# Optimization experiments

Hardware: AMD Instinct MI355X
Metric: run time of the kernel (lower is better)

## Reference

```python
import jax, jax.numpy as jnp
import numpy as np

B, T, V, ION, N = 16, 32, 26, 8, 500
U, E, H = 64, 512, 512
CIN = V * ION + 1  # 209


def setup_inputs() -> dict:
    key = jax.random.key(0)
    ks = jax.random.split(key, 40)
    s = 0.05
    inp = {
        "location_index": jax.random.uniform(ks[0], (B, T, V, ION), jnp.float32),
        "peaks_location": jax.random.uniform(ks[1], (B, N), jnp.float32),
        "peaks_intensity": jax.random.uniform(ks[2], (B, N), jnp.float32),
        "aa_input": jax.random.randint(ks[3], (B, T), 0, V),
        "h0": jax.random.normal(ks[4], (1, B, H), jnp.float32) * 0.1,
        "c0": jax.random.normal(ks[5], (1, B, H), jnp.float32) * 0.1,
        "dsf": jnp.zeros((), jnp.float32),
        "conv1_w": jax.random.normal(ks[6], (U, CIN), jnp.float32) * s,
        "conv1_b": jnp.zeros((U,), jnp.float32),
        "conv2_w": jax.random.normal(ks[7], (2 * U, U), jnp.float32) * s,
        "conv2_b": jnp.zeros((2 * U,), jnp.float32),
        "conv3_w": jax.random.normal(ks[8], (4 * U, 2 * U), jnp.float32) * s,
        "conv3_b": jnp.zeros((4 * U,), jnp.float32),
        "fc1_w": jax.random.normal(ks[9], (2 * U, 4 * U), jnp.float32) * s,
        "fc1_b": jnp.zeros((2 * U,), jnp.float32),
        "fc2_w": jax.random.normal(ks[10], (U, 2 * U), jnp.float32) * s,
        "fc2_b": jnp.zeros((U,), jnp.float32),
        "bn0_g": jnp.ones((CIN,), jnp.float32), "bn0_b": jnp.zeros((CIN,), jnp.float32),
        "bn1_g": jnp.ones((U,), jnp.float32), "bn1_b": jnp.zeros((U,), jnp.float32),
        "bn2_g": jnp.ones((2 * U,), jnp.float32), "bn2_b": jnp.zeros((2 * U,), jnp.float32),
        "bn3_g": jnp.ones((4 * U,), jnp.float32), "bn3_b": jnp.zeros((4 * U,), jnp.float32),
        "bn4_g": jnp.ones((2 * U,), jnp.float32), "bn4_b": jnp.zeros((2 * U,), jnp.float32),
        "bn5_g": jnp.ones((U,), jnp.float32), "bn5_b": jnp.zeros((U,), jnp.float32),
        "emb": jax.random.normal(ks[11], (V, E), jnp.float32) * s,
        "w_ih": jax.random.normal(ks[12], (4 * H, E), jnp.float32) * s,
        "w_hh": jax.random.normal(ks[13], (4 * H, H), jnp.float32) * s,
        "b_ih": jnp.zeros((4 * H,), jnp.float32),
        "b_hh": jnp.zeros((4 * H,), jnp.float32),
        "out_w": jax.random.normal(ks[14], (V, U + H), jnp.float32) * s,
        "out_b": jnp.zeros((V,), jnp.float32),
    }
    return inp


def _bn(x, g, b):
    # training-mode batch norm (biased variance), matches default torch module mode
    axes = (0, 2) if x.ndim == 3 else (0,)
    shp = (1, -1, 1) if x.ndim == 3 else (1, -1)
    m = jnp.mean(x, axes, keepdims=True)
    v = jnp.var(x, axes, keepdims=True)
    return (x - m) / jnp.sqrt(v + 1e-5) * g.reshape(shp) + b.reshape(shp)


def _forward(location_index, peaks_location, peaks_intensity, aa_input, h0, c0, dsf,
             conv1_w, conv1_b, conv2_w, conv2_b, conv3_w, conv3_b,
             fc1_w, fc1_b, fc2_w, fc2_b,
             bn0_g, bn0_b, bn1_g, bn1_b, bn2_g, bn2_b, bn3_g, bn3_b, bn4_g, bn4_b, bn5_g, bn5_b,
             emb, w_ih, w_hh, b_ih, b_hh, out_w, out_b):
    relu = jax.nn.relu
    pl = peaks_location[:, None, :, None]            # [B,1,N,1]
    pi = peaks_intensity[:, None, :, None]           # [B,1,N,1]
    li = location_index.reshape(B, T, 1, V * ION)    # [B,T,1,208]
    mp = (pl > 1e-5).astype(jnp.float32)
    ml = (li > 1e-5).astype(jnp.float32)
    ppm = (pl - li) / (li + 1e-6) * 1e6              # [B,T,N,208]
    feat = jnp.exp(-jnp.abs(ppm / 5.0 * jax.nn.sigmoid(dsf))) * mp * ml
    pi_b = jnp.broadcast_to(pi, (B, T, N, 1))
    x = jnp.concatenate([feat, pi_b], axis=3)        # [B,T,N,209]
    x = x.reshape(B * T, N, CIN).transpose(0, 2, 1)  # [BT,209,N]
    # TNet (1x1 convs are channel matmuls)
    x = _bn(x, bn0_g, bn0_b)
    x = relu(_bn(jnp.einsum('mcn,oc->mon', x, conv1_w) + conv1_b[:, None], bn1_g, bn1_b))
    x = relu(_bn(jnp.einsum('mcn,oc->mon', x, conv2_w) + conv2_b[:, None], bn2_g, bn2_b))
    x = relu(_bn(jnp.einsum('mcn,oc->mon', x, conv3_w) + conv3_b[:, None], bn3_g, bn3_b))
    x = jnp.max(x, axis=2)                            # [BT,4U]
    x = relu(_bn(x @ fc1_w.T + fc1_b, bn4_g, bn4_b))
    x = relu(_bn(x @ fc2_w.T + fc2_b, bn5_g, bn5_b))
    ion = x.reshape(B, T, U)
    # LSTM over aa embeddings (torch gate order i,f,g,o)
    xemb = emb[aa_input]                              # [B,T,E]
    def step(carry, xt):
        h, c = carry
        g = xt @ w_ih.T + b_ih + h @ w_hh.T + b_hh
        i, f, gg, o = jnp.split(g, 4, axis=1)
        c = jax.nn.sigmoid(f) * c + jax.nn.sigmoid(i) * jnp.tanh(gg)
        h = jax.nn.sigmoid(o) * jnp.tanh(c)
        return (h, c), h
    (hT, cT), hs = jax.lax.scan(step, (h0[0], c0[0]), xemb.transpose(1, 0, 2))
    lstm_out = hs.transpose(1, 0, 2)                  # [B,T,H]
    of = jnp.concatenate([ion, relu(lstm_out)], axis=2)  # dropout = identity (eval)
    logit = of @ out_w.T + out_b                      # [B,T,26]
    return logit, hT[None], cT[None]


def reference(location_index, peaks_location, peaks_intensity, aa_input, h0, c0, dsf,
              conv1_w, conv1_b, conv2_w, conv2_b, conv3_w, conv3_b,
              fc1_w, fc1_b, fc2_w, fc2_b,
              bn0_g, bn0_b, bn1_g, bn1_b, bn2_g, bn2_b, bn3_g, bn3_b, bn4_g, bn4_b, bn5_g, bn5_b,
              emb, w_ih, w_hh, b_ih, b_hh, out_w, out_b):
    return _forward(location_index, peaks_location, peaks_intensity, aa_input, h0, c0, dsf,
                    conv1_w, conv1_b, conv2_w, conv2_b, conv3_w, conv3_b,
                    fc1_w, fc1_b, fc2_w, fc2_b,
                    bn0_g, bn0_b, bn1_g, bn1_b, bn2_g, bn2_b, bn3_g, bn3_b, bn4_g, bn4_b, bn5_g, bn5_b,
                    emb, w_ih, w_hh, b_ih, b_hh, out_w, out_b)
```

## Files before the change

### kernel.cpp

```cpp
#include <hip/hip_runtime.h>
#include <hip/hip_bf16.h>
#include <math.h>

#define Bb 16
#define Tt 32
#define Vv 26
#define Nn 500
#define Uu 64
#define Hh 512
#define CIN 209
#define K1P 256
#define Mm 512
#define Rr 256000
#define NB1 4000
#define NB23 2000

typedef short short8 __attribute__((ext_vector_type(8)));
typedef float f32x4 __attribute__((ext_vector_type(4)));

__device__ __forceinline__ float sigf(float x){ return 1.0f/(1.0f+expf(-x)); }
__device__ __forceinline__ float frcp(float x){ return __builtin_amdgcn_rcpf(x); }
__device__ __forceinline__ unsigned short f2bf(float f){
  __hip_bfloat16 h = __float2bfloat16(f);
  return *reinterpret_cast<unsigned short*>(&h);
}
__device__ __forceinline__ float bf2f(unsigned short h){
  return __uint_as_float(((unsigned)h)<<16);
}

__global__ void k_front(const float* __restrict__ W2, const float* __restrict__ W3,
                        const float* __restrict__ EMB, const float* __restrict__ WIH,
                        const float* __restrict__ BIH, const float* __restrict__ BHH,
                        const float* __restrict__ L, const float* __restrict__ PL,
                        const float* __restrict__ PI, const float* __restrict__ DSF,
                        unsigned short* __restrict__ W2B, unsigned short* __restrict__ W3B,
                        unsigned short* __restrict__ W1B,
                        float* __restrict__ embw, float* __restrict__ ps0){
  int bid = blockIdx.x;
  int tid = threadIdx.x;
  if (bid < 172){
    int idx = bid*256 + tid;
    if (idx < 8192){ W2B[idx] = f2bf(W2[idx]); return; }
    idx -= 8192;
    if (idx < 32768){ W3B[idx] = f2bf(W3[idx]); return; }
    idx -= 32768;
    if (idx < 3008){ int oo = idx/47, kk = 209 + idx - (idx/47)*47; W1B[oo*K1P + kk] = 0; }
    return;
  }
  if (bid < 13484){
    int gw = (bid-172)*4 + (tid>>6);
    int lane = tid & 63;
    int v = gw >> 11;
    int j = gw & 2047;
    const float4* ea = (const float4*)&EMB[(size_t)v*512];
    const float4* wa = (const float4*)&WIH[(size_t)j*512];
    float4 e0 = ea[lane*2], e1 = ea[lane*2+1];
    float4 w0 = wa[lane*2], w1 = wa[lane*2+1];
    float s = e0.x*w0.x + e0.y*w0.y + e0.z*w0.z + e0.w*w0.w
            + e1.x*w1.x + e1.y*w1.y + e1.z*w1.z + e1.w*w1.w;
    #pragma unroll
    for (int off=1; off<64; off<<=1) s += __shfl_xor(s,off);
    if (lane==0) embw[(size_t)v*2048 + j] = s + BIH[j] + BHH[j];
    return;
  }
  int fid = bid - 13484;
  int m = fid>>3, q = fid&7;
  int b = m >> 5;
  int n0 = q*62 + ((q<4)?q:4);
  int cnt = 62 + (q<4 ? 1 : 0);
  __shared__ float pl_sh[63], pi_sh[63];
  for (int n=tid; n<cnt; n+=256){ pl_sh[n]=PL[b*Nn+n0+n]; pi_sh[n]=PI[b*Nn+n0+n]; }
  __syncthreads();
  if (tid >= CIN) return;
  float sum=0.f, sq=0.f;
  if (tid < CIN-1){
    float li = L[m*208 + tid];
    if (li > 1e-5f){
      float cfac = sigf(DSF[0])*200000.0f;
      float si = frcp(li + 1e-6f)*cfac;
      for (int n=0;n<cnt;n++){
        float pl = pl_sh[n];
        float f = (pl > 1e-5f) ? __expf(-fabsf((pl-li)*si)) : 0.f;
        sum += f; sq += f*f;
      }
    }
  } else {
    for (int n=0;n<cnt;n++){ float v=pi_sh[n]; sum+=v; sq+=v*v; }
  }
  int pb = m*8+q;
  ps0[(size_t)pb*CIN + tid] = sum;
  ps0[(size_t)(4096+pb)*CIN + tid] = sq;
}

__global__ void k_reduce0(const float* __restrict__ ps, const float* __restrict__ g,
                          const float* __restrict__ w1, unsigned short* __restrict__ w1b){
  int c = blockIdx.x;
  int tid = threadIdx.x;
  float s=0.f, q=0.f;
  for (int nb=tid; nb<4096; nb+=256){
    s += ps[(size_t)nb*CIN + c];
    q += ps[(size_t)(4096+nb)*CIN + c];
  }
  #pragma unroll
  for (int off=1; off<64; off<<=1){ s += __shfl_xor(s,off); q += __shfl_xor(q,off); }
  __shared__ float rs[4], rq[4];
  __shared__ float a_sh;
  if ((tid&63)==0){ rs[tid>>6]=s; rq[tid>>6]=q; }
  __syncthreads();
  if (tid==0){
    s = rs[0]+rs[1]+rs[2]+rs[3]; q = rq[0]+rq[1]+rq[2]+rq[3];
    float mean = s/(float)Rr;
    float var  = q/(float)Rr - mean*mean;
    a_sh = g[c]*rsqrtf(var + 1e-5f);
  }
  __syncthreads();
  if (tid < 64) w1b[tid*K1P + c] = f2bf(w1[tid*CIN + c] * a_sh);
}

__global__ void k_reduce_ps(const float* __restrict__ ps, int NB, int C, float invCount,
                            const float* __restrict__ g, const float* __restrict__ bt,
                            float* __restrict__ abb){
  int c = blockIdx.x;
  int tid = threadIdx.x;
  float s=0.f, q=0.f;
  for (int nb=tid; nb<NB; nb+=256){
    s += ps[(size_t)nb*C + c];
    q += ps[(size_t)(NB+nb)*C + c];
  }
  #pragma unroll
  for (int off=1; off<64; off<<=1){ s += __shfl_xor(s,off); q += __shfl_xor(q,off); }
  __shared__ float rs[4], rq[4];
  if ((tid&63)==0){ rs[tid>>6]=s; rq[tid>>6]=q; }
  __syncthreads();
  if (tid==0){
    s = rs[0]+rs[1]+rs[2]+rs[3]; q = rq[0]+rq[1]+rq[2]+rq[3];
    float mean = s*invCount;
    float var  = q*invCount - mean*mean;
    float istd = rsqrtf(var + 1e-5f);
    float a = g[c]*istd;
    abb[c] = a;
    abb[C+c] = bt[c] - mean*a;
  }
}

__global__ void k_colstats_par(const float* __restrict__ Z, int Mrows, int C,
                               const float* __restrict__ g, const float* __restrict__ bt,
                               float* __restrict__ abb){
  int c = blockIdx.x;
  int tid = threadIdx.x;
  float s=0.f,q=0.f;
  for (int r=tid; r<Mrows; r+=256){ float v=Z[(size_t)r*C+c]; s+=v; q+=v*v; }
  #pragma unroll
  for (int off=1; off<64; off<<=1){ s += __shfl_xor(s,off); q += __shfl_xor(q,off); }
  __shared__ float rs[4], rq[4];
  if ((tid&63)==0){ rs[tid>>6]=s; rq[tid>>6]=q; }
  __syncthreads();
  if (tid==0){
    s = rs[0]+rs[1]+rs[2]+rs[3]; q = rq[0]+rq[1]+rq[2]+rq[3];
    float mean = s/(float)Mrows;
    float var  = q/(float)Mrows - mean*mean;
    float istd = rsqrtf(var + 1e-5f);
    float a = g[c]*istd;
    abb[c]=a; abb[C+c]=bt[c]-mean*a;
  }
}

__launch_bounds__(256)
__global__ void k_conv1mf(const float* __restrict__ L, const float* __restrict__ PL,
                          const float* __restrict__ PI, const float* __restrict__ DSF,
                          const unsigned short* __restrict__ W1B,
                          unsigned short* __restrict__ Z1B, float* __restrict__ ps){
  __shared__ __align__(16) unsigned short Abuf[64*128];
  __shared__ __align__(16) unsigned short Bbuf[64*128];
  __shared__ __align__(16) float si_s[2][208];
  __shared__ float pl_s[64], pi_s[64];
  __shared__ int mi_i[64];
  __shared__ float red[4][2][64];
  int tid = threadIdx.x;
  int r0 = blockIdx.x*64;
  int m0 = r0/500, m1 = (r0+63)/500;
  float cfac = sigf(DSF[0])*200000.0f;
  if (tid < 64){
    int r = r0+tid; int m = r/500; int n = r - m*500; int b = m >> 5;
    pl_s[tid] = PL[b*Nn+n]; pi_s[tid] = PI[b*Nn+n]; mi_i[tid] = (m == m0) ? 0 : 1;
  }
  for (int j=tid; j<416; j+=256){
    int gg = (j>=208) ? 1 : 0; int jj = j - gg*208;
    float li = L[(size_t)(gg?m1:m0)*208 + jj];
    si_s[gg][jj] = (li > 1e-5f) ? frcp(li+1e-6f)*cfac : -1.0f;
  }
  int lane = tid&63, wid = tid>>6;
  int l15 = lane&15, lhi = lane>>4;
  int ar = wid*16 + l15;
  unsigned aswz = ((unsigned)(ar&7))<<4;
  f32x4 acc[4] = {};
  __syncthreads();
  for (int kc=0; kc<2; kc++){
    if (kc) __syncthreads();
    for (int e=tid; e<1024; e+=256){
      int row = e>>4; int k4 = (e&15)*8;
      short8 w = *(const short8*)&W1B[row*K1P + kc*128 + k4];
      unsigned byte = ((unsigned)(row*128 + k4))*2u ^ (((unsigned)(row&7))<<4);
      *(short8*)((char*)Bbuf + byte) = w;
    }
    for (int e=tid; e<1024; e+=256){
      int row = e>>4; int j0l = (e&15)*8;
      int jg = kc*128 + j0l;
      float pl = pl_s[row];
      bool plok = pl > 1e-5f;
      short8 st;
      if (jg < 208){
        int mi = mi_i[row];
        const float* lp = &L[(size_t)(mi?m1:m0)*208 + jg];
        float4 la = *(const float4*)lp;
        float4 lb = *(const float4*)(lp+4);
        float4 sa = *(const float4*)&si_s[mi][jg];
        float4 sb = *(const float4*)&si_s[mi][jg+4];
        float li[8] = {la.x,la.y,la.z,la.w,lb.x,lb.y,lb.z,lb.w};
        float si[8] = {sa.x,sa.y,sa.z,sa.w,sb.x,sb.y,sb.z,sb.w};
        #pragma unroll
        for (int j=0;j<8;j++){
          float v = (plok && si[j] >= 0.f) ? __expf(-fabsf((pl-li[j])*si[j])) : 0.f;
          st[j] = (short)f2bf(v);
        }
      } else {
        #pragma unroll
        for (int j=0;j<8;j++) st[j] = 0;
        if (jg == 208) st[0] = (short)f2bf(pi_s[row]);
      }
      unsigned byte = ((unsigned)(row*128 + j0l))*2u ^ (((unsigned)(row&7))<<4);
      *(short8*)((char*)Abuf + byte) = st;
    }
    __syncthreads();
    #pragma unroll
    for (int ks=0; ks<4; ks++){
      int kb = ks*32 + lhi*8;
      short8 af = *(const short8*)((const char*)Abuf + ((((unsigned)(ar*128 + kb))*2u) ^ aswz));
      #pragma unroll
      for (int fj=0; fj<4; fj++){
        int bc = fj*16 + l15;
        short8 bfv = *(const short8*)((const char*)Bbuf + ((((unsigned)(bc*128 + kb))*2u) ^ (((unsigned)(bc&7))<<4)));
        acc[fj] = __builtin_amdgcn_mfma_f32_16x16x32_bf16(af, bfv, acc[fj], 0, 0, 0);
      }
    }
  }
  #pragma unroll
  for (int fj=0; fj<4; fj++){
    int ch = fj*16 + l15;
    float s=0.f, q=0.f;
    #pragma unroll
    for (int qi=0; qi<4; qi++){
      float zv = acc[fj][qi];
      int rg = r0 + wid*16 + lhi*4 + qi;
      Z1B[(size_t)rg*Uu + ch] = f2bf(zv);
      s += zv; q = fmaf(zv,zv,q);
    }
    s += __shfl_xor(s,16); s += __shfl_xor(s,32);
    q += __shfl_xor(q,16); q += __shfl_xor(q,32);
    if (lhi == 0){ red[wid][0][ch]=s; red[wid][1][ch]=q; }
  }
  __syncthreads();
  if (tid < 64){
    float s = red[0][0][tid]+red[1][0][tid]+red[2][0][tid]+red[3][0][tid];
    float q = red[0][1][tid]+red[1][1][tid]+red[2][1][tid]+red[3][1][tid];
    ps[(size_t)blockIdx.x*Uu + tid] = s;
    ps[(size_t)(NB1 + blockIdx.x)*Uu + tid] = q;
  }
}

__launch_bounds__(256,4)
__global__ void k_convmf(const unsigned short* __restrict__ Xin, const float* __restrict__ abbIn,
                         const unsigned short* __restrict__ Wb,
                         unsigned short* __restrict__ Zout,
                         float* __restrict__ ps, int NB){
  constexpr int K = 64, Ctot = 128;
  __shared__ __align__(16) unsigned short Abuf[128*K];
  __shared__ float abbs[2*K];
  __shared__ float redS[2][128], redQ[2][128];
  int tid = threadIdx.x;
  int r0 = blockIdx.x*128;
  for (int e=tid; e<2*K; e+=256) abbs[e] = abbIn[e];
  __syncthreads();
  constexpr int CPR = K/8;
  for (int e=tid; e<128*CPR; e+=256){
    int row = e/CPR; int kc = (e - row*CPR)*8;
    short8 rawv = *(const short8*)(Xin + (size_t)(r0+row)*K + kc);
    short8 st;
    #pragma unroll
    for (int j=0;j<8;j++){
      float t = fmaxf(abbs[kc+j]*bf2f((unsigned short)rawv[j]) + abbs[K+kc+j], 0.f);
      st[j] = (short)f2bf(t);
    }
    unsigned byte = ((unsigned)(row*K + kc))*2u; byte ^= ((unsigned)(row&7))<<4;
    *(short8*)((char*)Abuf + byte) = st;
  }
  __syncthreads();

  int lane = tid&63, wid = tid>>6;
  int wr = wid>>1, wc = wid&1;
  int l15 = lane&15, lhi = lane>>4;
  f32x4 acc[4][4] = {};
  #pragma unroll
  for (int ks=0; ks<K/32; ks++){
    short8 af[4], bfr[4];
    int kb = ks*32 + lhi*8;
    #pragma unroll
    for (int f=0; f<4; f++){
      int arr = wr*64 + f*16 + l15;
      unsigned ab = ((unsigned)(arr*K + kb))*2u ^ (((unsigned)(arr&7))<<4);
      af[f] = *(const short8*)((const char*)Abuf + ab);
      int bc = wc*64 + f*16 + l15;
      bfr[f] = *(const short8*)&Wb[(size_t)bc*K + kb];
    }
    #pragma unroll
    for (int fi=0; fi<4; fi++)
      #pragma unroll
      for (int fj=0; fj<4; fj++)
        acc[fi][fj] = __builtin_amdgcn_mfma_f32_16x16x32_bf16(af[fi], bfr[fj], acc[fi][fj], 0, 0, 0);
  }

  #pragma unroll
  for (int fj=0; fj<4; fj++){
    int cg = wc*64 + fj*16 + l15;
    float s=0.f, q=0.f;
    #pragma unroll
    for (int fi=0; fi<4; fi++){
      #pragma unroll
      for (int qi=0; qi<4; qi++){
        float zv = acc[fi][fj][qi];
        int rg = r0 + wr*64 + fi*16 + lhi*4 + qi;
        Zout[(size_t)rg*Ctot + cg] = f2bf(zv);
        s += zv; q = fmaf(zv,zv,q);
      }
    }
    s += __shfl_xor(s,16); s += __shfl_xor(s,32);
    q += __shfl_xor(q,16); q += __shfl_xor(q,32);
    if (lhi == 0){ redS[wr][cg]=s; redQ[wr][cg]=q; }
  }
  __syncthreads();
  if (tid < 128){
    float s = redS[0][tid]+redS[1][tid];
    float q = redQ[0][tid]+redQ[1][tid];
    size_t ci = (size_t)blockIdx.x*Ctot + tid;
    ps[ci] = s;
    ps[(size_t)NB*Ctot + ci] = q;
  }
}

__launch_bounds__(256,3)
__global__ void k_conv3mf(const unsigned short* __restrict__ Xin, const float* __restrict__ abbIn,
                          const unsigned short* __restrict__ Wb,
                          float* __restrict__ ps, int NB,
                          float* __restrict__ pm, float* __restrict__ pn){
  constexpr int K = 128, Ctot = 256;
  __shared__ __align__(16) unsigned short Abuf[128*K];
  __shared__ float abbs[2*K];
  __shared__ float redS[2][128], redQ[2][128];
  __shared__ float mxS[2][2][128], mnS[2][2][128];
  int tid = threadIdx.x;
  int r0 = blockIdx.x*128;
  for (int e=tid; e<2*K; e+=256) abbs[e] = abbIn[e];
  __syncthreads();
  constexpr int CPR = K/8;
  for (int e=tid; e<128*CPR; e+=256){
    int row = e/CPR; int kc = (e - row*CPR)*8;
    short8 rawv = *(const short8*)(Xin + (size_t)(r0+row)*K + kc);
    short8 st;
    #pragma unroll
    for (int j=0;j<8;j++){
      float t = fmaxf(abbs[kc+j]*bf2f((unsigned short)rawv[j]) + abbs[K+kc+j], 0.f);
      st[j] = (short)f2bf(t);
    }
    unsigned byte = ((unsigned)(row*K + kc))*2u; byte ^= ((unsigned)(row&7))<<4;
    *(short8*)((char*)Abuf + byte) = st;
  }
  __syncthreads();

  int lane = tid&63, wid = tid>>6;
  int wr = wid>>1, wc = wid&1;
  int l15 = lane&15, lhi = lane>>4;
  int m0 = r0/500;
  int mhi = (m0+1)*500;
  bool onem = (r0+127) < mhi;

  for (int half=0; half<2; half++){
    int c0 = half*128;
    if (half) __syncthreads();

    f32x4 acc[4][4] = {};
    #pragma unroll
    for (int ks=0; ks<K/32; ks++){
      short8 af[4], bfr[4];
      int kb = ks*32 + lhi*8;
      #pragma unroll
      for (int f=0; f<4; f++){
        int arr = wr*64 + f*16 + l15;
        unsigned ab = ((unsigned)(arr*K + kb))*2u ^ (((unsigned)(arr&7))<<4);
        af[f] = *(const short8*)((const char*)Abuf + ab);
        int bc = c0 + wc*64 + f*16 + l15;
        bfr[f] = *(const short8*)&Wb[(size_t)bc*K + kb];
      }
      #pragma unroll
      for (int fi=0; fi<4; fi++)
        #pragma unroll
        for (int fj=0; fj<4; fj++)
          acc[fi][fj] = __builtin_amdgcn_mfma_f32_16x16x32_bf16(af[fi], bfr[fj], acc[fi][fj], 0, 0, 0);
    }

    if (onem){
      #pragma unroll
      for (int fj=0; fj<4; fj++){
        float s=0.f, q=0.f, mx0=-INFINITY, mn0=INFINITY;
        #pragma unroll
        for (int fi=0; fi<4; fi++){
          #pragma unroll
          for (int qi=0; qi<4; qi++){
            float zv = acc[fi][fj][qi];
            s += zv; q = fmaf(zv,zv,q);
            mx0 = fmaxf(mx0,zv); mn0 = fminf(mn0,zv);
          }
        }
        s += __shfl_xor(s,16); s += __shfl_xor(s,32);
        q += __shfl_xor(q,16); q += __shfl_xor(q,32);
        mx0 = fmaxf(mx0, __shfl_xor(mx0,16)); mx0 = fmaxf(mx0, __shfl_xor(mx0,32));
        mn0 = fminf(mn0, __shfl_xor(mn0,16)); mn0 = fminf(mn0, __shfl_xor(mn0,32));
        if (lhi == 0){
          int ch = wc*64 + fj*16 + l15;
          redS[wr][ch]=s; redQ[wr][ch]=q;
          mxS[wr][0][ch]=mx0; mxS[wr][1][ch]=-INFINITY;
          mnS[wr][0][ch]=mn0; mnS[wr][1][ch]=INFINITY;
        }
      }
    } else {
      #pragma unroll
      for (int fj=0; fj<4; fj++){
        float s=0.f, q=0.f;
        float mx0=-INFINITY,mx1=-INFINITY,mn0=INFINITY,mn1=INFINITY;
        #pragma unroll
        for (int fi=0; fi<4; fi++){
          #pragma unroll
          for (int qi=0; qi<4; qi++){
            float zv = acc[fi][fj][qi];
            int rg = r0 + wr*64 + fi*16 + lhi*4 + qi;
            s += zv; q = fmaf(zv,zv,q);
            if (rg >= mhi){ mx1=fmaxf(mx1,zv); mn1=fminf(mn1,zv); }
            else          { mx0=fmaxf(mx0,zv); mn0=fminf(mn0,zv); }
          }
        }
        s += __shfl_xor(s,16); s += __shfl_xor(s,32);
        q += __shfl_xor(q,16); q += __shfl_xor(q,32);
        mx0 = fmaxf(mx0, __shfl_xor(mx0,16)); mx0 = fmaxf(mx0, __shfl_xor(mx0,32));
        mx1 = fmaxf(mx1, __shfl_xor(mx1,16)); mx1 = fmaxf(mx1, __shfl_xor(mx1,32));
        mn0 = fminf(mn0, __shfl_xor(mn0,16)); mn0 = fminf(mn0, __shfl_xor(mn0,32));
        mn1 = fminf(mn1, __shfl_xor(mn1,16)); mn1 = fminf(mn1, __shfl_xor(mn1,32));
        if (lhi == 0){
          int ch = wc*64 + fj*16 + l15;
          redS[wr][ch]=s; redQ[wr][ch]=q;
          mxS[wr][0][ch]=mx0; mxS[wr][1][ch]=mx1;
          mnS[wr][0][ch]=mn0; mnS[wr][1][ch]=mn1;
        }
      }
    }
    __syncthreads();
    if (tid < 128){
      float s = redS[0][tid]+redS[1][tid];
      float q = redQ[0][tid]+redQ[1][tid];
      size_t ci = (size_t)blockIdx.x*Ctot + c0 + tid;
      ps[ci] = s;
      ps[(size_t)NB*Ctot + ci] = q;
      #pragma unroll
      for (int g=0; g<2; g++){
        pm[((size_t)blockIdx.x*2+g)*Ctot + c0 + tid] = fmaxf(mxS[0][g][tid], mxS[1][g][tid]);
        pn[((size_t)blockIdx.x*2+g)*Ctot + c0 + tid] = fminf(mnS[0][g][tid], mnS[1][g][tid]);
      }
    }
  }
}

__launch_bounds__(256)
__global__ void k_poolfc1(const float* __restrict__ pm, const float* __restrict__ pn,
                          const float* __restrict__ abb3, const float* __restrict__ FC1W,
                          float* __restrict__ Z4){
  __shared__ float of[256];
  int r = blockIdx.x;
  int tid = threadIdx.x;
  {
    int c = tid;
    int bxlo = (500*r)/128;
    int bxhi = (500*r+499)/128;
    float mx=-INFINITY, mn=INFINITY;
    for (int bx=bxlo; bx<=bxhi; bx++){
      int mb = (bx*128)/500;
      int gg = r - mb;
      if (gg==0 || gg==1){
        mx = fmaxf(mx, pm[((size_t)bx*2+gg)*256 + c]);
        mn = fminf(mn, pn[((size_t)bx*2+gg)*256 + c]);
      }
    }
    float a = abb3[c], bb = abb3[256+c];
    float zv = (a >= 0.f) ? mx : mn;
    of[c] = fmaxf(a*zv + bb, 0.f);
  }
  __syncthreads();
  if (tid < 128){
    float acc = 0.f;
    const float* wr = &FC1W[(size_t)tid*256];
    #pragma unroll 4
    for (int k=0;k<256;k++) acc = fmaf(of[k], wr[k], acc);
    Z4[(size_t)r*128 + tid] = acc;
  }
}

__launch_bounds__(256)
__global__ void k_fc(const float* __restrict__ A, const float* __restrict__ W,
                     const float* __restrict__ abb, float* __restrict__ C,
                     int Ncols, int K){
  int gw = blockIdx.x*4 + (threadIdx.x>>6);
  int lane = threadIdx.x & 63;
  int r = gw / Ncols, c = gw - r*Ncols;
  float s = 0.f;
  for (int k=lane; k<K; k+=64){
    float v = A[(size_t)r*K + k];
    if (abb) v = fmaxf(abb[k]*v + abb[K+k], 0.f);
    s = fmaf(v, W[(size_t)c*K + k], s);
  }
  #pragma unroll
  for (int off=1; off<64; off<<=1) s += __shfl_xor(s,off);
  if (lane==0) C[(size_t)r*Ncols + c] = s;
}

__launch_bounds__(256)
__global__ void k_lstm_step(const float* __restrict__ hprev, float* __restrict__ hnext,
                            const float* __restrict__ cin, float* __restrict__ cout,
                            const float* __restrict__ embw, const int* __restrict__ aa,
                            const float* __restrict__ whh, float* __restrict__ lout,
                            float* __restrict__ outhc, int t){
  __shared__ float h_s[16][516];
  __shared__ float g_s[4][16];
  int tid = threadIdx.x;
  int u = blockIdx.x;
  for (int e=tid; e<2048; e+=256){
    int idx = e*4;
    *(float4*)&h_s[idx>>9][idx&511] = *(const float4*)&hprev[idx];
  }
  __syncthreads();
  int w = tid>>6, lane = tid&63;
  int seg = lane>>4, b = lane&15;
  int j = w*512 + u;
  const float4* wrow = (const float4*)&whh[(size_t)j*512] + seg*32;
  const float4* hrow = (const float4*)&h_s[b][0] + seg*32;
  float a0=0.f, a1=0.f, a2=0.f, a3=0.f;
  #pragma unroll 4
  for (int k=0;k<32;k++){
    float4 wv = wrow[k]; float4 hv = hrow[k];
    a0 = fmaf(hv.x,wv.x,a0); a1 = fmaf(hv.y,wv.y,a1);
    a2 = fmaf(hv.z,wv.z,a2); a3 = fmaf(hv.w,wv.w,a3);
  }
  float s = (a0+a1)+(a2+a3);
  s += __shfl_xor(s,16);
  s += __shfl_xor(s,32);
  if (lane < 16){
    int v = aa[lane*Tt + t];
    g_s[w][lane] = s + embw[(size_t)v*2048 + j];
  }
  __syncthreads();
  if (tid < 16){
    int b2 = tid;
    float iv = g_s[0][b2], fv = g_s[1][b2], gv = g_s[2][b2], ov = g_s[3][b2];
    int ci = b2*512 + u;
    float cn = sigf(fv)*cin[ci] + sigf(iv)*tanhf(gv);
    float hn = sigf(ov)*tanhf(cn);
    cout[ci]=cn; hnext[ci]=hn;
    lout[(size_t)(b2*Tt + t)*Hh + u] = hn;
    if (outhc){ outhc[Mm*Vv + ci] = hn; outhc[Mm*Vv + Bb*Hh + ci] = cn; }
  }
}

__launch_bounds__(256)
__global__ void k_logits(const float* __restrict__ Z5, const float* __restrict__ abb5,
                         const float* __restrict__ lout, const float* __restrict__ outw,
                         const float* __restrict__ outb, float* __restrict__ out){
  __shared__ float of[576];
  int r = blockIdx.x;
  int tid = threadIdx.x;
  if (tid < 64) of[tid] = fmaxf(abb5[tid]*Z5[(size_t)r*64+tid] + abb5[64+tid], 0.f);
  for (int e=tid; e<512; e+=256) of[64+e] = fmaxf(lout[(size_t)r*512+e], 0.f);
  __syncthreads();
  int o = tid>>3, k0 = tid&7;
  if (o < Vv){
    float acc = 0.f;
    for (int k=k0; k<576; k+=8) acc = fmaf(of[k], outw[o*576+k], acc);
    acc += __shfl_xor(acc,1); acc += __shfl_xor(acc,2); acc += __shfl_xor(acc,4);
    if (k0==0) out[r*Vv + o] = acc + outb[o];
  }
}

extern "C" void kernel_launch(void* const* d_in, const int* in_sizes, int n_in,
                              void* d_out, int out_size, void* d_ws, size_t ws_size,
                              hipStream_t stream){
  (void)in_sizes; (void)n_in; (void)out_size; (void)ws_size;
  const float* L   = (const float*)d_in[0];
  const float* PL  = (const float*)d_in[1];
  const float* PI  = (const float*)d_in[2];
  const int*   AA  = (const int*)d_in[3];
  const float* H0  = (const float*)d_in[4];
  const float* C0  = (const float*)d_in[5];
  const float* DSF = (const float*)d_in[6];
  const float* W1  = (const float*)d_in[7];
  const float* W2  = (const float*)d_in[9];
  const float* W3  = (const float*)d_in[11];
  const float* FC1W= (const float*)d_in[13];
  const float* FC2W= (const float*)d_in[15];
  const float* G0=(const float*)d_in[17]; const float* Bt0=(const float*)d_in[18];
  const float* G1=(const float*)d_in[19]; const float* Bt1=(const float*)d_in[20];
  const float* G2=(const float*)d_in[21]; const float* Bt2=(const float*)d_in[22];
  const float* G3=(const float*)d_in[23]; const float* Bt3=(const float*)d_in[24];
  const float* G4=(const float*)d_in[25]; const float* Bt4=(const float*)d_in[26];
  const float* G5=(const float*)d_in[27]; const float* Bt5=(const float*)d_in[28];
  const float* EMB=(const float*)d_in[29];
  const float* WIH=(const float*)d_in[30];
  const float* WHH=(const float*)d_in[31];
  const float* BIH=(const float*)d_in[32];
  const float* BHH=(const float*)d_in[33];
  const float* OUTW=(const float*)d_in[34];
  const float* OUTB=(const float*)d_in[35];
  float* out = (float*)d_out;
  float* ws  = (float*)d_ws;

  size_t o = 0;
  unsigned short* Z1B = (unsigned short*)(ws+o); o += (size_t)Rr*32;
  unsigned short* Z2B = (unsigned short*)(ws+o); o += (size_t)Rr*64;
  float* PS0   = ws+o; o += 2*4096*CIN + 16;
  float* PS1   = ws+o; o += 2*NB1*64 + 16;
  float* PS2   = ws+o; o += 2*NB23*128 + 16;
  float* PS3   = ws+o; o += 2*NB23*256 + 16;
  float* PM3   = ws+o; o += NB23*2*256 + 16;
  float* PN3   = ws+o; o += NB23*2*256 + 16;
  float* ABB1  = ws+o; o += 128;
  float* ABB2  = ws+o; o += 256;
  float* ABB3  = ws+o; o += 512;
  float* ABB4  = ws+o; o += 256;
  float* ABB5  = ws+o; o += 128;
  unsigned short* W1B = (unsigned short*)(ws+o); o += 64*K1P/2 + 16;
  unsigned short* W2B = (unsigned short*)(ws+o); o += 4096 + 16;
  unsigned short* W3B = (unsigned short*)(ws+o); o += 16384 + 16;
  float* Z4    = ws+o; o += 65536;
  float* Z5    = ws+o; o += 32768;
  float* EMBW  = ws+o; o += 53248;
  float* HB0   = ws+o; o += 8192;
  float* HB1   = ws+o; o += 8192;
  float* CB    = ws+o; o += 8192;
  float* LOUT  = ws+o; o += 262144;

  k_front<<<17580,256,0,stream>>>(W2,W3,EMB,WIH,BIH,BHH,L,PL,PI,DSF,W2B,W3B,W1B,EMBW,PS0);

  k_reduce0<<<CIN,256,0,stream>>>(PS0,G0,W1,W1B);
  k_conv1mf<<<NB1,256,0,stream>>>(L,PL,PI,DSF,W1B,Z1B,PS1);
  k_reduce_ps<<<64,256,0,stream>>>(PS1, NB1, 64, 1.0f/(float)Rr, G1, Bt1, ABB1);
  k_convmf<<<NB23,256,0,stream>>>(Z1B,ABB1,W2B,Z2B,PS2,NB23);
  k_reduce_ps<<<128,256,0,stream>>>(PS2, NB23, 128, 1.0f/(float)Rr, G2, Bt2, ABB2);
  k_conv3mf<<<NB23,256,0,stream>>>(Z2B,ABB2,W3B,PS3,NB23,PM3,PN3);
  k_reduce_ps<<<256,256,0,stream>>>(PS3, NB23, 256, 1.0f/(float)Rr, G3, Bt3, ABB3);
  k_poolfc1<<<512,256,0,stream>>>(PM3,PN3,ABB3,FC1W,Z4);
  k_colstats_par<<<128,256,0,stream>>>(Z4,512,128,G4,Bt4,ABB4);
  k_fc<<<8192,256,0,stream>>>(Z4,FC2W,ABB4,Z5,64,128);
  k_colstats_par<<<64,256,0,stream>>>(Z5,512,64,G5,Bt5,ABB5);

  for (int t=0;t<32;t++){
    const float* hp = (t==0) ? H0 : ((t&1)?HB1:HB0);
    float* hn = (t&1)?HB0:HB1;
    const float* ci = (t==0) ? C0 : CB;
    float* outhc = (t==31) ? out : nullptr;
    k_lstm_step<<<512,256,0,stream>>>(hp,hn,ci,CB,EMBW,AA,WHH,LOUT,outhc,t);
  }

  k_logits<<<512,256,0,stream>>>(Z5,ABB5,LOUT,OUTW,OUTB,out);
}
```

Measured before the change: 420.4 us.

## Store LSTM recurrent weights as bf16 and process two hidden units per block

The front kernel converts W_hh to bf16 once. Each of the 32 LSTM step kernels then streams half as many weight bytes. The step kernel is reshaped to 512 threads handling two hidden units per block, so the h-state load into shared memory is amortised over twice the work. The cost is reduced precision of the recurrent weights, which compounds over 32 steps, plus an extra conversion pass over 1M elements in the front kernel.

```diff
diff --git a/kernel.cpp b/kernel.cpp
--- a/kernel.cpp
+++ b/kernel.cpp
@@ -29,26 +29,29 @@
 }
 
 __global__ void k_front(const float* __restrict__ W2, const float* __restrict__ W3,
+                        const float* __restrict__ WHH,
                         const float* __restrict__ EMB, const float* __restrict__ WIH,
                         const float* __restrict__ BIH, const float* __restrict__ BHH,
                         const float* __restrict__ L, const float* __restrict__ PL,
                         const float* __restrict__ PI, const float* __restrict__ DSF,
                         unsigned short* __restrict__ W2B, unsigned short* __restrict__ W3B,
-                        unsigned short* __restrict__ W1B,
+                        unsigned short* __restrict__ W1B, unsigned short* __restrict__ WHHB,
                         float* __restrict__ embw, float* __restrict__ ps0){
   int bid = blockIdx.x;
   int tid = threadIdx.x;
-  if (bid < 172){
+  if (bid < 4268){
     int idx = bid*256 + tid;
     if (idx < 8192){ W2B[idx] = f2bf(W2[idx]); return; }
     idx -= 8192;
     if (idx < 32768){ W3B[idx] = f2bf(W3[idx]); return; }
     idx -= 32768;
-    if (idx < 3008){ int oo = idx/47, kk = 209 + idx - (idx/47)*47; W1B[oo*K1P + kk] = 0; }
+    if (idx < 3008){ int oo = idx/47, kk = 209 + idx - (idx/47)*47; W1B[oo*K1P + kk] = 0; return; }
+    idx -= 3008;
+    if (idx < 1048576){ WHHB[idx] = f2bf(WHH[idx]); }
     return;
   }
-  if (bid < 13484){
-    int gw = (bid-172)*4 + (tid>>6);
+  if (bid < 17580){
+    int gw = (bid-4268)*4 + (tid>>6);
     int lane = tid & 63;
     int v = gw >> 11;
     int j = gw & 2047;
@@ -63,7 +66,7 @@
     if (lane==0) embw[(size_t)v*2048 + j] = s + BIH[j] + BHH[j];
     return;
   }
-  int fid = bid - 13484;
+  int fid = bid - 17580;
   int m = fid>>3, q = fid&7;
   int b = m >> 5;
   int n0 = q*62 + ((q<4)?q:4);
@@ -529,34 +532,43 @@
   if (lane==0) C[(size_t)r*Ncols + c] = s;
 }
 
-__launch_bounds__(256)
+__launch_bounds__(512)
 __global__ void k_lstm_step(const float* __restrict__ hprev, float* __restrict__ hnext,
                             const float* __restrict__ cin, float* __restrict__ cout,
                             const float* __restrict__ embw, const int* __restrict__ aa,
-                            const float* __restrict__ whh, float* __restrict__ lout,
+                            const unsigned short* __restrict__ whhb, float* __restrict__ lout,
                             float* __restrict__ outhc, int t){
   __shared__ float h_s[16][516];
-  __shared__ float g_s[4][16];
-  int tid = threadIdx.x;
-  int u = blockIdx.x;
-  for (int e=tid; e<2048; e+=256){
+  __shared__ float g_s[8][16];
+  int tid = threadIdx.x;
+  int u0 = blockIdx.x*2;
+  for (int e=tid; e<2048; e+=512){
     int idx = e*4;
     *(float4*)&h_s[idx>>9][idx&511] = *(const float4*)&hprev[idx];
   }
   __syncthreads();
   int w = tid>>6, lane = tid&63;
+  int ul = w>>2, gate = w&3;
   int seg = lane>>4, b = lane&15;
-  int j = w*512 + u;
-  const float4* wrow = (const float4*)&whh[(size_t)j*512] + seg*32;
-  const float4* hrow = (const float4*)&h_s[b][0] + seg*32;
-  float a0=0.f, a1=0.f, a2=0.f, a3=0.f;
-  #pragma unroll 4
-  for (int k=0;k<32;k++){
-    float4 wv = wrow[k]; float4 hv = hrow[k];
-    a0 = fmaf(hv.x,wv.x,a0); a1 = fmaf(hv.y,wv.y,a1);
-    a2 = fmaf(hv.z,wv.z,a2); a3 = fmaf(hv.w,wv.w,a3);
-  }
-  float s = (a0+a1)+(a2+a3);
+  int j = gate*512 + u0 + ul;
+  const short8* wrow = (const short8*)&whhb[(size_t)j*512 + seg*128];
+  const float* hrow = &h_s[b][seg*128];
+  float a0=0.f, a1=0.f;
+  #pragma unroll
+  for (int k=0;k<16;k++){
+    short8 wv = wrow[k];
+    const float4* hp4 = (const float4*)(hrow + k*8);
+    float4 h0 = hp4[0], h1 = hp4[1];
+    a0 = fmaf(h0.x, bf2f((unsigned short)wv[0]), a0);
+    a1 = fmaf(h0.y, bf2f((unsigned short)wv[1]), a1);
+    a0 = fmaf(h0.z, bf2f((unsigned short)wv[2]), a0);
+    a1 = fmaf(h0.w, bf2f((unsigned short)wv[3]), a1);
+    a0 = fmaf(h1.x, bf2f((unsigned short)wv[4]), a0);
+    a1 = fmaf(h1.y, bf2f((unsigned short)wv[5]), a1);
+    a0 = fmaf(h1.z, bf2f((unsigned short)wv[6]), a0);
+    a1 = fmaf(h1.w, bf2f((unsigned short)wv[7]), a1);
+  }
+  float s = a0 + a1;
   s += __shfl_xor(s,16);
   s += __shfl_xor(s,32);
   if (lane < 16){
@@ -564,14 +576,15 @@
     g_s[w][lane] = s + embw[(size_t)v*2048 + j];
   }
   __syncthreads();
-  if (tid < 16){
-    int b2 = tid;
-    float iv = g_s[0][b2], fv = g_s[1][b2], gv = g_s[2][b2], ov = g_s[3][b2];
-    int ci = b2*512 + u;
+  if (tid < 32){
+    int ul2 = tid>>4, b2 = tid&15;
+    float iv = g_s[ul2*4+0][b2], fv = g_s[ul2*4+1][b2];
+    float gv = g_s[ul2*4+2][b2], ov = g_s[ul2*4+3][b2];
+    int ci = b2*512 + u0 + ul2;
     float cn = sigf(fv)*cin[ci] + sigf(iv)*tanhf(gv);
     float hn = sigf(ov)*tanhf(cn);
     cout[ci]=cn; hnext[ci]=hn;
-    lout[(size_t)(b2*Tt + t)*Hh + u] = hn;
+    lout[(size_t)(b2*Tt + t)*Hh + u0 + ul2] = hn;
     if (outhc){ outhc[Mm*Vv + ci] = hn; outhc[Mm*Vv + Bb*Hh + ci] = cn; }
   }
 }
@@ -644,6 +657,7 @@
   unsigned short* W1B = (unsigned short*)(ws+o); o += 64*K1P/2 + 16;
   unsigned short* W2B = (unsigned short*)(ws+o); o += 4096 + 16;
   unsigned short* W3B = (unsigned short*)(ws+o); o += 16384 + 16;
+  unsigned short* WHHB = (unsigned short*)(ws+o); o += 524288 + 16;
   float* Z4    = ws+o; o += 65536;
   float* Z5    = ws+o; o += 32768;
   float* EMBW  = ws+o; o += 53248;
@@ -652,7 +666,8 @@
   float* CB    = ws+o; o += 8192;
   float* LOUT  = ws+o; o += 262144;
 
-  k_front<<<17580,256,0,stream>>>(W2,W3,EMB,WIH,BIH,BHH,L,PL,PI,DSF,W2B,W3B,W1B,EMBW,PS0);
+  k_front<<<21676,256,0,stream>>>(W2,W3,WHH,EMB,WIH,BIH,BHH,L,PL,PI,DSF,
+                                  W2B,W3B,W1B,WHHB,EMBW,PS0);
 
   k_reduce0<<<CIN,256,0,stream>>>(PS0,G0,W1,W1B);
   k_conv1mf<<<NB1,256,0,stream>>>(L,PL,PI,DSF,W1B,Z1B,PS1);
@@ -671,7 +686,7 @@
     float* hn = (t&1)?HB0:HB1;
     const float* ci = (t==0) ? C0 : CB;
     float* outhc = (t==31) ? out : nullptr;
-    k_lstm_step<<<512,256,0,stream>>>(hp,hn,ci,CB,EMBW,AA,WHH,LOUT,outhc,t);
+    k_lstm_step<<<256,512,0,stream>>>(hp,hn,ci,CB,EMBW,AA,WHHB,LOUT,outhc,t);
   }
 
   k_logits<<<512,256,0,stream>>>(Z5,ABB5,LOUT,OUTW,OUTB,out);
```

Result: faster. 391.2 us (-6.9%).
